# Performance work log

Hardware: AMD Instinct MI355X
Metric: run time of the kernel (lower is better)

## Reference

```python
import jax, jax.numpy as jnp
import numpy as np

B, T, I, H, L, S = 128, 256, 256, 256, 4, 3


def _gru(x_t, w_i, b_i, b_h):
    # torch.nn.GRUCell called WITHOUT hx in the source => hidden state is 0,
    # so Whh @ 0 vanishes and only the b_hh bias contributes to the gates.
    gi = x_t @ w_i.T + b_i                      # [B, 3H]
    hh = b_h.shape[0] // 3
    i_r, i_z, i_n = gi[:, :hh], gi[:, hh:2 * hh], gi[:, 2 * hh:]
    h_r, h_z, h_n = b_h[:hh], b_h[hh:2 * hh], b_h[2 * hh:]
    r = jax.nn.sigmoid(i_r + h_r)
    z = jax.nn.sigmoid(i_z + h_z)
    n = jnp.tanh(i_n + r * h_n)
    return (1.0 - z) * n                        # + z * 0


def setup_inputs() -> dict:
    key = jax.random.key(0)
    ks = jax.random.split(key, 12)
    s = 1.0 / np.sqrt(H)
    u = lambda k, shape: jax.random.uniform(k, shape, jnp.float32, -s, s)
    return {
        "x": jax.random.normal(ks[0], (B, T, I), jnp.float32),
        "hidden": jax.random.normal(ks[1], (B, L, L), jnp.float32),
        "w_ih0": u(ks[2], (S, 3 * H, I)),      # layer-0 input weights, per split
        "b_ih0": u(ks[3], (S, 3 * H)),
        "b_hh0": u(ks[4], (S, 3 * H)),
        "w_ih": u(ks[5], (S, L - 1, 3 * H, H)),  # layers 1..L-1
        "b_ih": u(ks[6], (S, L - 1, 3 * H)),
        "b_hh": u(ks[7], (S, L - 1, 3 * H)),
        "w_lw": u(ks[8], (L, H)),              # layer_weights: Linear(H -> L)
        "b_lw": u(ks[9], (L,)),
        "w_sel": u(ks[10], (S, H + I)),        # selective_layer: Linear(H+I -> S)
        "b_sel": u(ks[11], (S,)),
    }


def reference(x, hidden, w_ih0, b_ih0, b_hh0, w_ih, b_ih, b_hh, w_lw, b_lw, w_sel, b_sel):
    Lm1 = w_ih.shape[1]

    def run_stack(x_t, cur):
        # cur is a (possibly traced) int index selecting one of S GRU stacks
        hs = [_gru(x_t, w_ih0[cur], b_ih0[cur], b_hh0[cur])]
        for l in range(Lm1):
            hs.append(_gru(hs[-1], w_ih[cur, l], b_ih[cur, l], b_hh[cur, l]))
        return jnp.stack(hs, axis=1)            # [B, L, H]

    h0 = run_stack(x[:, 0, :], 0)               # first step always uses stack 0

    def step(h, x_t):
        energy = h @ w_lw.T + b_lw              # [B, L, L]
        attn = jnp.sum(hidden * energy, axis=2) # [B, L]
        a = jax.nn.softmax(attn, axis=1)
        ctx = jnp.einsum('bl,blh->bh', a, h)    # [B, H]
        scores = jnp.concatenate([ctx, x_t], axis=1) @ w_sel.T + b_sel  # [B, S]
        cur = jnp.argmax(jnp.sum(scores, axis=0))  # batch-summed routing
        h_new = run_stack(x_t, cur)
        return h_new, h_new[:, -1, :]

    h_final, ys = jax.lax.scan(step, h0, jnp.swapaxes(x[:, 1:, :], 0, 1))
    outputs = jnp.concatenate([h0[:, -1:, :], jnp.swapaxes(ys, 0, 1)], axis=1)  # [B, T, H]
    return outputs, h_final[:, -1, :]
```

## Files before the change

### kernel.cpp

```cpp
#include <hip/hip_runtime.h>
#include <math.h>

#define Bsz 128
#define Tsz 256
#define Isz 256
#define Hsz 256
#define Lsz 4
#define Ssz 3
#define Mrows (Bsz*Tsz)

using f16x8 = __attribute__((ext_vector_type(8))) _Float16;
using f32x4 = __attribute__((ext_vector_type(4))) float;

#define LOG2E 1.44269504f

__global__ __launch_bounds__(256) void f32_to_f16(
    const float* __restrict__ src, _Float16* __restrict__ dst, int n8)
{
  const int idx = blockIdx.x * 256 + threadIdx.x;
  if (idx >= n8) return;
  const float4 v0 = *(const float4*)(src + (size_t)idx * 8);
  const float4 v1 = *(const float4*)(src + (size_t)idx * 8 + 4);
  _Float16 h[8];
  h[0] = (_Float16)v0.x; h[1] = (_Float16)v0.y;
  h[2] = (_Float16)v0.z; h[3] = (_Float16)v0.w;
  h[4] = (_Float16)v1.x; h[5] = (_Float16)v1.y;
  h[6] = (_Float16)v1.z; h[7] = (_Float16)v1.w;
  *(uint4*)(dst + (size_t)idx * 8) = *(uint4*)h;
}

__global__ __launch_bounds__(256, 2) void gemm_gru_f16(
    const _Float16* __restrict__ Abase, size_t a_cur_stride,
    const _Float16* __restrict__ Wbase, size_t w_cur_stride,
    const float* __restrict__ bi_g, size_t bi_stride,
    const float* __restrict__ bh_g, size_t bh_stride,
    _Float16* __restrict__ Hout)
{
  __shared__ _Float16 AhS[3][8192];

  const int tid  = threadIdx.x;
  const int cu   = blockIdx.z;
  const int n0   = blockIdx.y * 64;
  const int rmb  = blockIdx.x * 512;

  const _Float16* A = Abase + (size_t)cu * a_cur_stride;
  const _Float16* W = Wbase + (size_t)cu * w_cur_stride;
  const float* bi = bi_g + (size_t)cu * bi_stride;
  const float* bh = bh_g + (size_t)cu * bh_stride;

  const int lane = tid & 63;
  const int wv   = tid >> 6;
  const int q    = lane >> 4;
  const int c    = lane & 15;

  const int ncol = n0 + wv * 16 + c;
  f16x8 wf[3][8];
  #pragma unroll
  for (int s = 0; s < 3; s++)
    #pragma unroll
    for (int k0 = 0; k0 < 8; k0++)
      wf[s][k0] = *(const f16x8*)(W + (size_t)(s * 256 + ncol) * 256 + k0 * 32 + q * 8);
  #pragma unroll
  for (int s = 0; s < 3; s++)
    #pragma unroll
    for (int k0 = 0; k0 < 8; k0++)
      asm volatile("" : "+v"(wf[s][k0]));

  const float c0  = -LOG2E * (bi[ncol] + bh[ncol]);
  const float c1  =  LOG2E * (bi[256 + ncol] + bh[256 + ncol]);
  const float c3  = 2.f * LOG2E * bi[512 + ncol];
  const float bhn = bh[512 + ncol];

  f32x4 acc[3][2];

  auto stage = [&](int buf, int ch) {
    const int rm = rmb + ch * 32;
    #pragma unroll
    for (int i = 0; i < 4; i++) {
      const int p0 = 8 * wv + 2 * i;
      const int pk = p0 + (lane >> 5);
      const _Float16* src = A + (size_t)(rm + (lane & 31)) * 256 + pk * 8;
      __builtin_amdgcn_global_load_lds(
          (const __attribute__((address_space(1))) void*)src,
          (__attribute__((address_space(3))) void*)&AhS[buf][p0 * 256],
          16, 0, 0);
    }
  };

  auto compute_chunk = [&](int buf, int ch) {
    const int rm = rmb + ch * 32;
    #pragma unroll
    for (int s = 0; s < 3; s++)
      #pragma unroll
      for (int mi = 0; mi < 2; mi++)
        acc[s][mi] = (f32x4)0.f;
    #pragma unroll
    for (int k0 = 0; k0 < 8; k0++) {
      const f16x8 a0 = *(const f16x8*)&AhS[buf][(k0 * 4 + q) * 256 + c * 8];
      const f16x8 a1 = *(const f16x8*)&AhS[buf][(k0 * 4 + q) * 256 + 128 + c * 8];
      #pragma unroll
      for (int s = 0; s < 3; s++) {
        acc[s][0] = __builtin_amdgcn_mfma_f32_16x16x32_f16(a0, wf[s][k0], acc[s][0], 0, 0, 0);
        acc[s][1] = __builtin_amdgcn_mfma_f32_16x16x32_f16(a1, wf[s][k0], acc[s][1], 0, 0, 0);
      }
    }
    #pragma unroll
    for (int mi = 0; mi < 2; mi++) {
      #pragma unroll
      for (int reg = 0; reg < 4; reg++) {
        const float ar = acc[0][mi][reg];
        const float az = acc[1][mi][reg];
        const float an = acc[2][mi][reg];
        const float e0 = __builtin_amdgcn_exp2f(fmaf(-LOG2E, ar, c0));
        const float r  = __builtin_amdgcn_rcpf(1.f + e0);
        const float e1 = __builtin_amdgcn_exp2f(fmaf(LOG2E, az, c1));
        const float tt = fmaf(r, bhn, an);
        const float a2 = fminf(fmaf(2.f * LOG2E, tt, c3), 120.f);
        const float e2 = __builtin_amdgcn_exp2f(a2);
        const float out = (e2 - 1.f) *
            __builtin_amdgcn_rcpf((1.f + e1) * (1.f + e2));
        const size_t row = (size_t)cu * Mrows + rm + mi * 16 + q * 4 + reg;
        Hout[row * 256 + ncol] = (_Float16)out;
      }
    }
  };

  stage(0, 0);
  stage(1, 1);
  asm volatile("s_waitcnt vmcnt(4)" ::: "memory");
  __builtin_amdgcn_s_barrier();

  int bc = 0;
  for (int t = 0; t < 14; ++t) {
    int bs = bc + 2; if (bs >= 3) bs -= 3;
    stage(bs, t + 2);
    compute_chunk(bc, t);
    asm volatile("s_waitcnt vmcnt(12)" ::: "memory");
    __builtin_amdgcn_s_barrier();
    bc = (bc + 1 == 3) ? 0 : bc + 1;
  }
  compute_chunk(bc, 14);
  asm volatile("s_waitcnt vmcnt(0)" ::: "memory");
  __builtin_amdgcn_s_barrier();
  bc = (bc + 1 == 3) ? 0 : bc + 1;
  compute_chunk(bc, 15);
}

__global__ __launch_bounds__(256) void ep_tile(
    const _Float16* __restrict__ Hh,
    const float* __restrict__ w_lw, const float* __restrict__ w_sel, int layer,
    float* __restrict__ e, float* __restrict__ p)
{
  __shared__ _Float16 hs[64 * 264];
  __shared__ float wc[7][256];
  __shared__ float ps[4][64][8];
  const int tid = threadIdx.x;
  const size_t mg0 = (size_t)blockIdx.x * 64;

  #pragma unroll
  for (int i = 0; i < 8; i++) {
    const int ci = tid + i * 256;
    const int row = ci >> 5, kc = ci & 31;
    *(uint4*)&hs[row * 264 + kc * 8] =
        *(const uint4*)(Hh + (mg0 + row) * 256 + kc * 8);
  }
  #pragma unroll
  for (int j = 0; j < 7; j++)
    wc[j][tid] = (j < 4) ? w_lw[j * 256 + tid] : w_sel[(j - 4) * 512 + tid];
  __syncthreads();

  const int r = tid & 63, pp = tid >> 6;
  float acc[7] = {0.f, 0.f, 0.f, 0.f, 0.f, 0.f, 0.f};
  #pragma unroll
  for (int i = 0; i < 8; i++) {
    union { uint4 u; _Float16 h[8]; } hv;
    hv.u = *(uint4*)&hs[r * 264 + pp * 64 + i * 8];
    float hf[8];
    #pragma unroll
    for (int k = 0; k < 8; k++) hf[k] = (float)hv.h[k];
    #pragma unroll
    for (int j = 0; j < 7; j++) {
      const float4 w0 = *(const float4*)&wc[j][pp * 64 + i * 8];
      const float4 w1 = *(const float4*)&wc[j][pp * 64 + i * 8 + 4];
      acc[j] += hf[0] * w0.x + hf[1] * w0.y + hf[2] * w0.z + hf[3] * w0.w
              + hf[4] * w1.x + hf[5] * w1.y + hf[6] * w1.z + hf[7] * w1.w;
    }
  }
  #pragma unroll
  for (int j = 0; j < 7; j++) ps[pp][r][j] = acc[j];
  __syncthreads();

  if (tid < 64) {
    float d[7];
    #pragma unroll
    for (int j = 0; j < 7; j++)
      d[j] = ps[0][tid][j] + ps[1][tid][j] + ps[2][tid][j] + ps[3][tid][j];
    const size_t mg = mg0 + tid;
    const int cc = (int)(mg >> 15);
    const int m  = (int)(mg & 32767);
    const int b = m >> 8, t = m & 255;
    const size_t base = ((size_t)cc * Tsz + t) * Bsz + b;
    #pragma unroll
    for (int j = 0; j < 4; j++) e[base * 16 + layer * 4 + j] = d[j];
    #pragma unroll
    for (int j = 0; j < 3; j++) p[base * 12 + layer * 3 + j] = d[4 + j];
  }
}

__global__ __launch_bounds__(128) void attn_finish(
    const float* __restrict__ e, const float* __restrict__ p,
    const float* __restrict__ hidden, const float* __restrict__ b_lw,
    float* __restrict__ score_h)
{
  const int t = blockIdx.x, cc = blockIdx.y;
  const int b = threadIdx.x;
  const float* eb = e + ((size_t)(cc * Tsz + t) * Bsz + b) * 16;
  const float* pb = p + ((size_t)(cc * Tsz + t) * Bsz + b) * 12;
  const float* hb = hidden + b * 16;
  const float bl0 = b_lw[0], bl1 = b_lw[1], bl2 = b_lw[2], bl3 = b_lw[3];
  float attn[4];
  #pragma unroll
  for (int i = 0; i < 4; i++) {
    attn[i] = hb[i * 4 + 0] * (eb[i * 4 + 0] + bl0)
            + hb[i * 4 + 1] * (eb[i * 4 + 1] + bl1)
            + hb[i * 4 + 2] * (eb[i * 4 + 2] + bl2)
            + hb[i * 4 + 3] * (eb[i * 4 + 3] + bl3);
  }
  const float mx = fmaxf(fmaxf(attn[0], attn[1]), fmaxf(attn[2], attn[3]));
  float ex[4], sum = 0.f;
  #pragma unroll
  for (int i = 0; i < 4; i++) { ex[i] = expf(attn[i] - mx); sum += ex[i]; }
  const float inv = 1.f / sum;
  float sc[3];
  #pragma unroll
  for (int s = 0; s < 3; s++) {
    float v = 0.f;
    #pragma unroll
    for (int i = 0; i < 4; i++) v += ex[i] * pb[i * 3 + s];
    sc[s] = v * inv;
  }
  #pragma unroll
  for (int off = 32; off; off >>= 1)
    #pragma unroll
    for (int s = 0; s < 3; s++) sc[s] += __shfl_xor(sc[s], off);
  __shared__ float red[2][3];
  const int wv = threadIdx.x >> 6, ln = threadIdx.x & 63;
  if (ln == 0) { red[wv][0] = sc[0]; red[wv][1] = sc[1]; red[wv][2] = sc[2]; }
  __syncthreads();
  if (threadIdx.x == 0) {
    #pragma unroll
    for (int s = 0; s < 3; s++)
      score_h[((size_t)cc * Tsz + t) * 3 + s] = red[0][s] + red[1][s];
  }
}

__global__ __launch_bounds__(256) void xs_kernel(
    const float* __restrict__ x, const float* __restrict__ w_sel,
    const float* __restrict__ b_sel, float* __restrict__ xs)
{
  const int t = blockIdx.x, k = threadIdx.x;
  float s = 0.f;
  for (int b = 0; b < Bsz; b++) s += x[((size_t)b * Tsz + t) * Isz + k];
  float pr[3];
  #pragma unroll
  for (int qq = 0; qq < 3; qq++) pr[qq] = s * w_sel[qq * (Hsz + Isz) + Hsz + k];
  #pragma unroll
  for (int off = 32; off; off >>= 1)
    #pragma unroll
    for (int qq = 0; qq < 3; qq++) pr[qq] += __shfl_xor(pr[qq], off);
  __shared__ float red[4][3];
  const int wv = k >> 6, ln = k & 63;
  if (ln == 0) { red[wv][0] = pr[0]; red[wv][1] = pr[1]; red[wv][2] = pr[2]; }
  __syncthreads();
  if (k == 0) {
    #pragma unroll
    for (int qq = 0; qq < 3; qq++)
      xs[t * 3 + qq] = red[0][qq] + red[1][qq] + red[2][qq] + red[3][qq]
                      + (float)Bsz * b_sel[qq];
  }
}

__global__ __launch_bounds__(256) void select_kernel(
    const float* __restrict__ score_h, const float* __restrict__ xs,
    int* __restrict__ cur)
{
  __shared__ int f[Tsz][3];
  const int tid = threadIdx.x;
  for (int u = tid; u < (Tsz - 1) * 3; u += 256) {
    const int t = 1 + u / 3, cc = u % 3;
    const float* sh = score_h + ((size_t)cc * Tsz + (t - 1)) * 3;
    const float* xr = xs + t * 3;
    const float v0 = sh[0] + xr[0];
    const float v1 = sh[1] + xr[1];
    const float v2 = sh[2] + xr[2];
    int best = 0; float bv = v0;
    if (v1 > bv) { bv = v1; best = 1; }
    if (v2 > bv) { bv = v2; best = 2; }
    f[t][cc] = best;
  }
  __syncthreads();
  if (tid == 0) {
    int cc = 0; cur[0] = 0;
    for (int t = 1; t < Tsz; t++) { cc = f[t][cc]; cur[t] = cc; }
  }
}

__global__ __launch_bounds__(256) void gather_out(
    const _Float16* __restrict__ Hh, const int* __restrict__ cur,
    float* __restrict__ out)
{
  const size_t idx = ((size_t)blockIdx.x * 256 + threadIdx.x) * 4;
  const size_t BTH = (size_t)Bsz * Tsz * Hsz;
  int b, t, h;
  if (idx < BTH) {
    b = (int)(idx >> 16);
    const int rem = (int)(idx & 65535);
    t = rem >> 8; h = rem & 255;
  } else {
    const size_t r2 = idx - BTH;
    b = (int)(r2 >> 8); h = (int)(r2 & 255); t = Tsz - 1;
  }
  const int cc = cur[t];
  const size_t g = (((size_t)cc * Mrows + (size_t)b * Tsz + t) * Hsz + h);
  union { ushort4 u; _Float16 hv[4]; } cv;
  cv.u = *(const ushort4*)(Hh + g);
  float4 v;
  v.x = (float)cv.hv[0]; v.y = (float)cv.hv[1];
  v.z = (float)cv.hv[2]; v.w = (float)cv.hv[3];
  *(float4*)(out + idx) = v;
}

extern "C" void kernel_launch(void* const* d_in, const int* in_sizes, int n_in,
                              void* d_out, int out_size, void* d_ws, size_t ws_size,
                              hipStream_t stream) {
  const float* x      = (const float*)d_in[0];
  const float* hidden = (const float*)d_in[1];
  const float* w_ih0  = (const float*)d_in[2];
  const float* b_ih0  = (const float*)d_in[3];
  const float* b_hh0  = (const float*)d_in[4];
  const float* w_ih   = (const float*)d_in[5];
  const float* b_ih   = (const float*)d_in[6];
  const float* b_hh   = (const float*)d_in[7];
  const float* w_lw   = (const float*)d_in[8];
  const float* b_lw   = (const float*)d_in[9];
  const float* w_sel  = (const float*)d_in[10];
  const float* b_sel  = (const float*)d_in[11];
  float* out = (float*)d_out;

  char* w = (char*)d_ws;
  const size_t HN = (size_t)3 * Mrows * 256;
  const size_t XN = (size_t)Bsz * Tsz * Isz;
  const size_t W0N = (size_t)3 * 768 * 256;
  const size_t WLN = (size_t)3 * 3 * 768 * 256;
  _Float16* HA  = (_Float16*)w; w += HN * 2;
  _Float16* HB  = (_Float16*)w; w += HN * 2;
  _Float16* xh  = (_Float16*)w; w += XN * 2;
  _Float16* Wh0 = (_Float16*)w; w += W0N * 2;
  _Float16* WhL = (_Float16*)w; w += WLN * 2;
  float* e       = (float*)w; w += (size_t)3 * Tsz * Bsz * 16 * 4;
  float* p       = (float*)w; w += (size_t)3 * Tsz * Bsz * 12 * 4;
  float* score_h = (float*)w; w += (size_t)3 * Tsz * 3 * 4;
  float* xsb     = (float*)w; w += (size_t)Tsz * 3 * 4;
  int*   curb    = (int*)w;   w += (size_t)Tsz * 4;

  f32_to_f16<<<(int)(XN / 8 + 255) / 256, 256, 0, stream>>>(x, xh, (int)(XN / 8));
  f32_to_f16<<<(int)(W0N / 8 + 255) / 256, 256, 0, stream>>>(w_ih0, Wh0, (int)(W0N / 8));
  f32_to_f16<<<(int)(WLN / 8 + 255) / 256, 256, 0, stream>>>(w_ih, WhL, (int)(WLN / 8));

  dim3 ggrid(64, 4, 3);

  gemm_gru_f16<<<ggrid, 256, 0, stream>>>(
      xh, (size_t)0, Wh0, (size_t)768 * 256,
      b_ih0, (size_t)768, b_hh0, (size_t)768, HA);
  ep_tile<<<(3 * Mrows) / 64, 256, 0, stream>>>(HA, w_lw, w_sel, 0, e, p);

  const size_t wcur = (size_t)3 * 768 * 256;
  const size_t bst  = (size_t)3 * 768;
  _Float16* ping = HA; _Float16* pong = HB;
  for (int l = 1; l < 4; l++) {
    gemm_gru_f16<<<ggrid, 256, 0, stream>>>(
        ping, (size_t)Mrows * 256,
        WhL + (size_t)(l - 1) * 768 * 256, wcur,
        b_ih + (size_t)(l - 1) * 768, bst,
        b_hh + (size_t)(l - 1) * 768, bst, pong);
    ep_tile<<<(3 * Mrows) / 64, 256, 0, stream>>>(pong, w_lw, w_sel, l, e, p);
    _Float16* t1 = ping; ping = pong; pong = t1;
  }

  attn_finish<<<dim3(Tsz, 3), 128, 0, stream>>>(e, p, hidden, b_lw, score_h);
  xs_kernel<<<Tsz, 256, 0, stream>>>(x, w_sel, b_sel, xsb);
  select_kernel<<<1, 256, 0, stream>>>(score_h, xsb, curb);
  gather_out<<<8224, 256, 0, stream>>>(ping, curb, out);
}
```

Baseline: 404.1 us.

## Fuse per-layer epilogue projections into next-layer GEMM and merge f16 conversions

The energy and selector projections for layers 0-2 are now computed inside the following layer's GEMM kernel. It reads the already-staged input tile from LDS, reduces across the four waves through shared memory, and accumulates into e/p with atomics. Three of the four ep_tile launches, and their re-reads of the hidden activations, go away; only the final layer keeps a separate pass. The three f32-to-f16 conversion launches are merged into one. The cost is extra registers, LDS and FMA work inside the GEMM, atomic traffic, memsets to zero the accumulators, and added lgkmcnt waits in the pipeline.

```diff
diff --git a/kernel.cpp b/kernel.cpp
--- a/kernel.cpp
+++ b/kernel.cpp
@@ -14,19 +14,24 @@
 
 #define LOG2E 1.44269504f
 
-__global__ __launch_bounds__(256) void f32_to_f16(
-    const float* __restrict__ src, _Float16* __restrict__ dst, int n8)
-{
-  const int idx = blockIdx.x * 256 + threadIdx.x;
-  if (idx >= n8) return;
-  const float4 v0 = *(const float4*)(src + (size_t)idx * 8);
-  const float4 v1 = *(const float4*)(src + (size_t)idx * 8 + 4);
+__global__ __launch_bounds__(256) void f32_to_f16_3(
+    const float* __restrict__ s0, _Float16* __restrict__ d0, int n0,
+    const float* __restrict__ s1, _Float16* __restrict__ d1, int n1,
+    const float* __restrict__ s2, _Float16* __restrict__ d2, int n2)
+{
+  int idx = blockIdx.x * 256 + threadIdx.x;
+  const float* s; _Float16* d;
+  if (idx < n0)           { s = s0; d = d0; }
+  else if (idx < n0 + n1) { idx -= n0; s = s1; d = d1; }
+  else                    { idx -= n0 + n1; if (idx >= n2) return; s = s2; d = d2; }
+  const float4 v0 = *(const float4*)(s + (size_t)idx * 8);
+  const float4 v1 = *(const float4*)(s + (size_t)idx * 8 + 4);
   _Float16 h[8];
   h[0] = (_Float16)v0.x; h[1] = (_Float16)v0.y;
   h[2] = (_Float16)v0.z; h[3] = (_Float16)v0.w;
   h[4] = (_Float16)v1.x; h[5] = (_Float16)v1.y;
   h[6] = (_Float16)v1.z; h[7] = (_Float16)v1.w;
-  *(uint4*)(dst + (size_t)idx * 8) = *(uint4*)h;
+  *(uint4*)(d + (size_t)idx * 8) = *(uint4*)h;
 }
 
 __global__ __launch_bounds__(256, 2) void gemm_gru_f16(
@@ -34,9 +39,12 @@
     const _Float16* __restrict__ Wbase, size_t w_cur_stride,
     const float* __restrict__ bi_g, size_t bi_stride,
     const float* __restrict__ bh_g, size_t bh_stride,
-    _Float16* __restrict__ Hout)
+    _Float16* __restrict__ Hout,
+    const float* __restrict__ w_lw, const float* __restrict__ w_sel,
+    float* __restrict__ e_out, float* __restrict__ p_out, int layer_ep)
 {
   __shared__ _Float16 AhS[3][8192];
+  __shared__ float PS[2][4][32][7];
 
   const int tid  = threadIdx.x;
   const int cu   = blockIdx.z;
@@ -70,6 +78,25 @@
   const float c1  =  LOG2E * (bi[256 + ncol] + bh[256 + ncol]);
   const float c3  = 2.f * LOG2E * bi[512 + ncol];
   const float bhn = bh[512 + ncol];
+
+  const int eprow = lane >> 1;
+  const int eppl  = blockIdx.y * 8 + wv * 2 + (lane & 1);
+  f16x8 wep[7];
+  if (layer_ep >= 0) {
+    #pragma unroll
+    for (int j = 0; j < 7; j++) {
+      const float* wsrc = (j < 4) ? (w_lw + j * 256 + eppl * 8)
+                                  : (w_sel + (size_t)(j - 4) * 512 + eppl * 8);
+      const float4 wa = *(const float4*)wsrc;
+      const float4 wb = *(const float4*)(wsrc + 4);
+      f16x8 wv8;
+      wv8[0] = (_Float16)wa.x; wv8[1] = (_Float16)wa.y;
+      wv8[2] = (_Float16)wa.z; wv8[3] = (_Float16)wa.w;
+      wv8[4] = (_Float16)wb.x; wv8[5] = (_Float16)wb.y;
+      wv8[6] = (_Float16)wb.z; wv8[7] = (_Float16)wb.w;
+      wep[j] = wv8;
+    }
+  }
 
   f32x4 acc[3][2];
 
@@ -102,6 +129,22 @@
       for (int s = 0; s < 3; s++) {
         acc[s][0] = __builtin_amdgcn_mfma_f32_16x16x32_f16(a0, wf[s][k0], acc[s][0], 0, 0, 0);
         acc[s][1] = __builtin_amdgcn_mfma_f32_16x16x32_f16(a1, wf[s][k0], acc[s][1], 0, 0, 0);
+      }
+    }
+    if (layer_ep >= 0) {
+      const f16x8 hv8 = *(const f16x8*)&AhS[buf][eppl * 256 + eprow * 8];
+      float pacc[7];
+      #pragma unroll
+      for (int j = 0; j < 7; j++) {
+        float a = 0.f;
+        #pragma unroll
+        for (int k = 0; k < 8; k++)
+          a = fmaf((float)hv8[k], (float)wep[j][k], a);
+        pacc[j] = a + __shfl_xor(a, 1);
+      }
+      if ((lane & 1) == 0) {
+        #pragma unroll
+        for (int j = 0; j < 7; j++) PS[ch & 1][wv][eprow][j] = pacc[j];
       }
     }
     #pragma unroll
@@ -125,6 +168,20 @@
     }
   };
 
+  auto ep_accum = [&](int pb, int ch) {
+    if (layer_ep < 0) return;
+    if (tid < 224) {
+      const int r = tid / 7, j = tid - r * 7;
+      const float v = PS[pb][0][r][j] + PS[pb][1][r][j]
+                    + PS[pb][2][r][j] + PS[pb][3][r][j];
+      const int m  = rmb + ch * 32 + r;
+      const int bb = m >> 8, ttim = m & 255;
+      const size_t base = ((size_t)cu * Tsz + ttim) * Bsz + bb;
+      if (j < 4) atomicAdd(&e_out[base * 16 + layer_ep * 4 + j], v);
+      else       atomicAdd(&p_out[base * 12 + layer_ep * 3 + (j - 4)], v);
+    }
+  };
+
   stage(0, 0);
   stage(1, 1);
   asm volatile("s_waitcnt vmcnt(4)" ::: "memory");
@@ -135,15 +192,19 @@
     int bs = bc + 2; if (bs >= 3) bs -= 3;
     stage(bs, t + 2);
     compute_chunk(bc, t);
-    asm volatile("s_waitcnt vmcnt(12)" ::: "memory");
+    asm volatile("s_waitcnt vmcnt(12) lgkmcnt(0)" ::: "memory");
     __builtin_amdgcn_s_barrier();
+    ep_accum(t & 1, t);
     bc = (bc + 1 == 3) ? 0 : bc + 1;
   }
   compute_chunk(bc, 14);
-  asm volatile("s_waitcnt vmcnt(0)" ::: "memory");
+  asm volatile("s_waitcnt vmcnt(0) lgkmcnt(0)" ::: "memory");
   __builtin_amdgcn_s_barrier();
-  bc = (bc + 1 == 3) ? 0 : bc + 1;
-  compute_chunk(bc, 15);
+  ep_accum(0, 14);
+  compute_chunk(0, 15);
+  asm volatile("s_waitcnt lgkmcnt(0)" ::: "memory");
+  __builtin_amdgcn_s_barrier();
+  ep_accum(1, 15);
 }
 
 __global__ __launch_bounds__(256) void ep_tile(
@@ -363,16 +424,20 @@
   float* xsb     = (float*)w; w += (size_t)Tsz * 3 * 4;
   int*   curb    = (int*)w;   w += (size_t)Tsz * 4;
 
-  f32_to_f16<<<(int)(XN / 8 + 255) / 256, 256, 0, stream>>>(x, xh, (int)(XN / 8));
-  f32_to_f16<<<(int)(W0N / 8 + 255) / 256, 256, 0, stream>>>(w_ih0, Wh0, (int)(W0N / 8));
-  f32_to_f16<<<(int)(WLN / 8 + 255) / 256, 256, 0, stream>>>(w_ih, WhL, (int)(WLN / 8));
+  hipMemsetAsync(e, 0, (size_t)3 * Tsz * Bsz * 16 * 4, stream);
+  hipMemsetAsync(p, 0, (size_t)3 * Tsz * Bsz * 12 * 4, stream);
+
+  f32_to_f16_3<<<5248, 256, 0, stream>>>(
+      x, xh, (int)(XN / 8),
+      w_ih0, Wh0, (int)(W0N / 8),
+      w_ih, WhL, (int)(WLN / 8));
 
   dim3 ggrid(64, 4, 3);
 
   gemm_gru_f16<<<ggrid, 256, 0, stream>>>(
       xh, (size_t)0, Wh0, (size_t)768 * 256,
-      b_ih0, (size_t)768, b_hh0, (size_t)768, HA);
-  ep_tile<<<(3 * Mrows) / 64, 256, 0, stream>>>(HA, w_lw, w_sel, 0, e, p);
+      b_ih0, (size_t)768, b_hh0, (size_t)768, HA,
+      nullptr, nullptr, nullptr, nullptr, -1);
 
   const size_t wcur = (size_t)3 * 768 * 256;
   const size_t bst  = (size_t)3 * 768;
@@ -382,10 +447,11 @@
         ping, (size_t)Mrows * 256,
         WhL + (size_t)(l - 1) * 768 * 256, wcur,
         b_ih + (size_t)(l - 1) * 768, bst,
-        b_hh + (size_t)(l - 1) * 768, bst, pong);
-    ep_tile<<<(3 * Mrows) / 64, 256, 0, stream>>>(pong, w_lw, w_sel, l, e, p);
+        b_hh + (size_t)(l - 1) * 768, bst, pong,
+        w_lw, w_sel, e, p, l - 1);
     _Float16* t1 = ping; ping = pong; pong = t1;
   }
+  ep_tile<<<(3 * Mrows) / 64, 256, 0, stream>>>(ping, w_lw, w_sel, 3, e, p);
 
   attn_finish<<<dim3(Tsz, 3), 128, 0, stream>>>(e, p, hidden, b_lw, score_h);
   xs_kernel<<<Tsz, 256, 0, stream>>>(x, w_sel, b_sel, xsb);
```

Result: slower. 460.5 us (+14.0%).
